# Kernel optimization log

Hardware: AMD Instinct MI355X
Metric: run time of the kernel (lower is better)

## Reference

```python
import jax, jax.numpy as jnp
import numpy as np

D_MODEL = 512
N_HEADS = 8
D_K = D_MODEL // N_HEADS


def setup_inputs() -> dict:
    key = jax.random.key(0)
    ks = jax.random.split(key, 11)
    B, L, D = 2, 4096, D_MODEL
    s = 1.0 / np.sqrt(D)
    return {
        "q": jax.random.normal(ks[0], (B, L, D), jnp.float32),
        "k": jax.random.normal(ks[1], (B, L, D), jnp.float32),
        "v": jax.random.normal(ks[2], (B, L, D), jnp.float32),
        "Wq": jax.random.normal(ks[3], (D, D), jnp.float32) * s,
        "bq": jnp.zeros((D,), jnp.float32),
        "Wk": jax.random.normal(ks[4], (D, D), jnp.float32) * s,
        "bk": jnp.zeros((D,), jnp.float32),
        "Wv": jax.random.normal(ks[5], (D, D), jnp.float32) * s,
        "bv": jnp.zeros((D,), jnp.float32),
        "Wo": jax.random.normal(ks[6], (D, D), jnp.float32) * s,
        "bo": jnp.zeros((D,), jnp.float32),
    }


def reference(q, k, v, Wq, bq, Wk, bk, Wv, bv, Wo, bo):
    B, L, D = q.shape
    H, dk = N_HEADS, D_K
    # projections -> [B, H, L, dk]
    qh = (q @ Wq + bq).reshape(B, L, H, dk).transpose(0, 2, 1, 3)
    kh = (k @ Wk + bk).reshape(B, -1, H, dk).transpose(0, 2, 1, 3)
    vh = (v @ Wv + bv).reshape(B, -1, H, dk).transpose(0, 2, 1, 3)
    scores = jnp.einsum("bhqd,bhkd->bhqk", qh, kh) / jnp.sqrt(jnp.float32(dk))
    attn = jax.nn.softmax(scores, axis=-1)  # dropout: eval-mode identity
    ctx = jnp.einsum("bhqk,bhkd->bhqd", attn, vh)
    ctx = ctx.transpose(0, 2, 1, 3).reshape(B, L, D)
    return ctx @ Wo + bo
```

## Files before the change

kernel.cpp:

```cpp
#include <hip/hip_runtime.h>
#include <hip/hip_bf16.h>

#define NB 2
#define NL 4096
#define ND 512
#define NH 8
#define NDK 64
#define NM (NB * NL)
#define QSCALE 0.18033688011112042f

typedef short bf16x8_t __attribute__((ext_vector_type(8)));
typedef float f32x4_t __attribute__((ext_vector_type(4)));

static __device__ __forceinline__ unsigned short f2bs(float f) {
  union { float f; unsigned u; } c; c.f = f;
  unsigned r = c.u + 0x7fffu + ((c.u >> 16) & 1u);
  return (unsigned short)(r >> 16);
}
static __device__ __forceinline__ float bs2f(unsigned short s) {
  union { unsigned u; float f; } c; c.u = ((unsigned)s) << 16; return c.f;
}
static __device__ __forceinline__ unsigned pk_bf16(float a, float b) {
  union { __hip_bfloat162 h; unsigned u; } c;
  c.h = __float22bfloat162_rn(make_float2(a, b));
  return c.u;
}
static __device__ __forceinline__ unsigned cvt_pk_hw(float a, float b) {
  unsigned r;
  asm("v_cvt_pk_bf16_f32 %0, %1, %2" : "=v"(r) : "v"(a), "v"(b));
  return r;
}

__global__ __launch_bounds__(256)
void round3_kernel(const float* __restrict__ s0, const float* __restrict__ s1,
                   const float* __restrict__ s2, unsigned short* __restrict__ d0,
                   unsigned short* __restrict__ d1, unsigned short* __restrict__ d2)
{
  const float* s = blockIdx.y == 0 ? s0 : (blockIdx.y == 1 ? s1 : s2);
  unsigned short* d = blockIdx.y == 0 ? d0 : (blockIdx.y == 1 ? d1 : d2);
  const size_t i = ((size_t)blockIdx.x * 256 + threadIdx.x) * 8;
  const float4 f0 = *(const float4*)(s + i);
  const float4 f1 = *(const float4*)(s + i + 4);
  uint4 o;
  o.x = pk_bf16(f0.x, f0.y);
  o.y = pk_bf16(f0.z, f0.w);
  o.z = pk_bf16(f1.x, f1.y);
  o.w = pk_bf16(f1.z, f1.w);
  *(uint4*)(d + i) = o;
}

struct WArgs {
  const float* W[4];
  unsigned short* Th[4];
  unsigned short* Tl[4];
};
__global__ __launch_bounds__(256)
void wsplit_kernel(WArgs a)
{
  const int z = blockIdx.z;
  const float* __restrict__ W = a.W[z];
  const int tid = threadIdx.x;
  const int n = blockIdx.x * 64 + (tid & 63);
  const int kb = blockIdx.y * 64 + (tid >> 6) * 16;
  unsigned short h[16], l[16];
#pragma unroll
  for (int u = 0; u < 16; ++u) {
    const float x = W[(size_t)(kb + u) * ND + n];
    h[u] = f2bs(x);
    l[u] = f2bs(x - bs2f(h[u]));
  }
  unsigned wh[8], wl[8];
#pragma unroll
  for (int p = 0; p < 8; ++p) {
    wh[p] = (unsigned)h[2 * p] | ((unsigned)h[2 * p + 1] << 16);
    wl[p] = (unsigned)l[2 * p] | ((unsigned)l[2 * p + 1] << 16);
  }
  unsigned short* th = a.Th[z] + (size_t)n * ND + kb;
  unsigned short* tl = a.Tl[z] + (size_t)n * ND + kb;
  *(uint4*)th = make_uint4(wh[0], wh[1], wh[2], wh[3]);
  *(uint4*)(th + 8) = make_uint4(wh[4], wh[5], wh[6], wh[7]);
  *(uint4*)tl = make_uint4(wl[0], wl[1], wl[2], wl[3]);
  *(uint4*)(tl + 8) = make_uint4(wl[4], wl[5], wl[6], wl[7]);
}

template <bool ASPLIT, int NJ, int OUTMODE>
__device__ __forceinline__ void gemm_core(
    const unsigned short* __restrict__ Ahi, const unsigned short* __restrict__ Alo,
    const unsigned short* __restrict__ Bh, const unsigned short* __restrict__ Bl,
    const float* __restrict__ bias, unsigned short* __restrict__ outH,
    float* __restrict__ outF, int m0, int n0, float scale)
{
  __shared__ unsigned short AH[128][36];
  __shared__ unsigned short AL[ASPLIT ? 128 : 1][36];
  __shared__ unsigned short BHs[NJ * 16][36];
  __shared__ unsigned short BLs[NJ * 16][36];

  const int tid = threadIdx.x;
  const int lane = tid & 63, w = tid >> 6;
  const int m = lane & 15, quad = lane >> 4;
  const int r = tid >> 1, hf = (tid & 1) * 16;
  const int rb = (NJ == 8) ? (tid >> 1) : (tid >> 2);
  const int cb = (NJ == 8) ? ((tid & 1) * 16) : ((tid & 3) * 8);

  const unsigned short* aRow = Ahi + (size_t)(m0 + r) * ND + hf;
  const unsigned short* alRow = ASPLIT ? (Alo + (size_t)(m0 + r) * ND + hf) : nullptr;
  const unsigned short* bhRow = Bh + (size_t)(n0 + rb) * ND + cb;
  const unsigned short* blRow = Bl + (size_t)(n0 + rb) * ND + cb;

  uint4 ra0 = *(const uint4*)(aRow);
  uint4 ra1 = *(const uint4*)(aRow + 8);
  uint4 rl0, rl1;
  if constexpr (ASPLIT) {
    rl0 = *(const uint4*)(alRow);
    rl1 = *(const uint4*)(alRow + 8);
  }
  uint4 rbh0 = *(const uint4*)(bhRow);
  uint4 rbl0 = *(const uint4*)(blRow);
  uint4 rbh1, rbl1;
  if constexpr (NJ == 8) {
    rbh1 = *(const uint4*)(bhRow + 8);
    rbl1 = *(const uint4*)(blRow + 8);
  }

  f32x4_t acc[2][NJ];
#pragma unroll
  for (int i = 0; i < 2; ++i)
#pragma unroll
    for (int j = 0; j < NJ; ++j) acc[i][j] = (f32x4_t){0.f, 0.f, 0.f, 0.f};

  for (int k0 = 0; k0 < ND; k0 += 32) {
    __syncthreads();
    *(uint4*)&AH[r][hf] = ra0;
    *(uint4*)&AH[r][hf + 8] = ra1;
    if constexpr (ASPLIT) {
      *(uint4*)&AL[r][hf] = rl0;
      *(uint4*)&AL[r][hf + 8] = rl1;
    }
    *(uint4*)&BHs[rb][cb] = rbh0;
    *(uint4*)&BLs[rb][cb] = rbl0;
    if constexpr (NJ == 8) {
      *(uint4*)&BHs[rb][cb + 8] = rbh1;
      *(uint4*)&BLs[rb][cb + 8] = rbl1;
    }
    if (k0 + 32 < ND) {
      const int kn = k0 + 32;
      ra0 = *(const uint4*)(aRow + kn);
      ra1 = *(const uint4*)(aRow + kn + 8);
      if constexpr (ASPLIT) {
        rl0 = *(const uint4*)(alRow + kn);
        rl1 = *(const uint4*)(alRow + kn + 8);
      }
      rbh0 = *(const uint4*)(bhRow + kn);
      rbl0 = *(const uint4*)(blRow + kn);
      if constexpr (NJ == 8) {
        rbh1 = *(const uint4*)(bhRow + kn + 8);
        rbl1 = *(const uint4*)(blRow + kn + 8);
      }
    }
    __syncthreads();

    bf16x8_t ah[2], al[2];
#pragma unroll
    for (int i = 0; i < 2; ++i) {
      ah[i] = *(const bf16x8_t*)&AH[w * 32 + 16 * i + m][quad * 8];
      if constexpr (ASPLIT) al[i] = *(const bf16x8_t*)&AL[w * 32 + 16 * i + m][quad * 8];
    }
#pragma unroll
    for (int j = 0; j < NJ; ++j) {
      const bf16x8_t bhj = *(const bf16x8_t*)&BHs[16 * j + m][quad * 8];
      const bf16x8_t blj = *(const bf16x8_t*)&BLs[16 * j + m][quad * 8];
#pragma unroll
      for (int i = 0; i < 2; ++i) {
        acc[i][j] = __builtin_amdgcn_mfma_f32_16x16x32_bf16(ah[i], bhj, acc[i][j], 0, 0, 0);
        acc[i][j] = __builtin_amdgcn_mfma_f32_16x16x32_bf16(ah[i], blj, acc[i][j], 0, 0, 0);
        if constexpr (ASPLIT)
          acc[i][j] = __builtin_amdgcn_mfma_f32_16x16x32_bf16(al[i], bhj, acc[i][j], 0, 0, 0);
      }
    }
  }

  if constexpr (OUTMODE == 1) {
#pragma unroll
    for (int i = 0; i < 2; ++i)
#pragma unroll
      for (int rr = 0; rr < 4; ++rr) {
        const int mg = m0 + w * 32 + 16 * i + quad * 4 + rr;
#pragma unroll
        for (int j = 0; j < NJ; ++j) {
          const int n = n0 + 16 * j + m;
          outF[(size_t)mg * ND + n] = (acc[i][j][rr] + bias[n]) * scale;
        }
      }
  } else if constexpr (OUTMODE == 0) {
    unsigned short* T = &BHs[0][0];
    const int bb = m0 >> 12;
#pragma unroll 1
    for (int p = 0; p < 4; ++p) {
      __syncthreads();
      if (w == p) {
#pragma unroll
        for (int i = 0; i < 2; ++i)
#pragma unroll
          for (int j = 0; j < NJ; ++j) {
            const int n = 16 * j + m;
            const float bv = bias[n0 + n];
#pragma unroll
            for (int rr = 0; rr < 4; ++rr)
              T[(16 * i + quad * 4 + rr) * 136 + n] =
                  f2bs((acc[i][j][rr] + bv) * scale);
          }
      }
      __syncthreads();
      const int lr = tid >> 3;
      const int seg = tid & 7;
      const uint4 t0 = *(const uint4*)&T[lr * 136 + seg * 16];
      const uint4 t1 = *(const uint4*)&T[lr * 136 + seg * 16 + 8];
      const int ng = n0 + seg * 16;
      const int h = ng >> 6, d = ng & (NDK - 1);
      const int l = (m0 + p * 32 + lr) & (NL - 1);
      unsigned short* dp = outH + (((size_t)(bb * NH + h)) * NL + l) * NDK + d;
      *(uint4*)dp = t0;
      *(uint4*)(dp + 8) = t1;
    }
  } else {
    unsigned short* T = &BHs[0][0];
    const int bb = m0 >> 12;
    const int lbase = m0 & (NL - 1);
#pragma unroll 1
    for (int p = 0; p < 4; ++p) {
      __syncthreads();
      if (w == p) {
#pragma unroll
        for (int i = 0; i < 2; ++i)
#pragma unroll
          for (int j = 0; j < NJ; ++j) {
            const int n = 16 * j + m;
            const float bv = bias[n0 + n];
            const unsigned w0 = pk_bf16((acc[i][j][0] + bv) * scale,
                                        (acc[i][j][1] + bv) * scale);
            const unsigned w1 = pk_bf16((acc[i][j][2] + bv) * scale,
                                        (acc[i][j][3] + bv) * scale);
            *(uint2*)&T[n * 34 + 16 * i + quad * 4] = make_uint2(w0, w1);
          }
      }
      __syncthreads();
      const int n = tid >> 1;
      const int l0 = (tid & 1) * 16;
      const uint4 t0 = *(const uint4*)&T[n * 34 + l0];
      const uint4 t1 = *(const uint4*)&T[n * 34 + l0 + 8];
      const int ng = n0 + n;
      const int h = ng >> 6, d = ng & (NDK - 1);
      unsigned short* dp =
          outH + (((size_t)(bb * NH + h)) * NDK + d) * NL + lbase + 32 * p + l0;
      *(uint4*)dp = t0;
      *(uint4*)(dp + 8) = t1;
    }
  }
}

struct ProjArgs {
  const unsigned short* A[3];
  const unsigned short* Bh[3];
  const unsigned short* Bl[3];
  const float* bias[3];
  unsigned short* out[3];
  float scale[3];
};
__global__ __launch_bounds__(256, 3)
void gemm_proj_kernel(ProjArgs a)
{
  const int z = blockIdx.z;
  if (z < 2)
    gemm_core<false, 8, 0>(a.A[z], nullptr, a.Bh[z], a.Bl[z], a.bias[z], a.out[z],
                           nullptr, blockIdx.x * 128, blockIdx.y * 128, a.scale[z]);
  else
    gemm_core<false, 8, 2>(a.A[2], nullptr, a.Bh[2], a.Bl[2], a.bias[2], a.out[2],
                           nullptr, blockIdx.x * 128, blockIdx.y * 128, a.scale[2]);
}
__global__ __launch_bounds__(256, 3)
void gemm_out_kernel(const unsigned short* __restrict__ Ahi,
                     const unsigned short* __restrict__ Alo,
                     const unsigned short* __restrict__ Bh,
                     const unsigned short* __restrict__ Bl,
                     const float* __restrict__ bias, float* __restrict__ out)
{
  gemm_core<true, 4, 1>(Ahi, Alo, Bh, Bl, bias, nullptr, out,
                        blockIdx.x * 128, blockIdx.y * 64, 1.0f);
}

__global__ __launch_bounds__(256, 2)
void attn_kernel(const unsigned short* __restrict__ qh, const unsigned short* __restrict__ kh,
                 const unsigned short* __restrict__ vt_g, float* __restrict__ op,
                 float* __restrict__ lp)
{
  __shared__ unsigned short Ks[2][64 * 64];
  __shared__ unsigned short Vt[2][64 * 64];

  const int tid = threadIdx.x;
  const int w = tid >> 6;
  const int lane = tid & 63;
  const int m = lane & 15;
  const int quad = lane >> 4;
  const int sw = m & 7;

  const int bid = blockIdx.x;
  const int half = bid & 1;
  const int qt = (bid >> 1) & 15;
  const int bh = bid >> 5;
  const int kt0 = half * 32, kt1 = kt0 + 32;
  const unsigned short* qb = qh + (size_t)bh * NL * NDK;
  const unsigned short* kb = kh + (size_t)bh * NL * NDK;
  const unsigned short* vb = vt_g + (size_t)bh * NDK * NL;

  bf16x8_t aq[4][2];
#pragma unroll
  for (int mt = 0; mt < 4; ++mt) {
    const unsigned short* qsrc =
        qb + (size_t)(qt * 256 + w * 64 + mt * 16 + m) * NDK + quad * 8;
    aq[mt][0] = *(const bf16x8_t*)(qsrc);
    aq[mt][1] = *(const bf16x8_t*)(qsrc + 32);
  }

  const short ob = (short)0x3F80;
  const bf16x8_t ones = {ob, ob, ob, ob, ob, ob, ob, ob};

  f32x4_t o[4][4];
#pragma unroll
  for (int mt = 0; mt < 4; ++mt)
#pragma unroll
    for (int nt = 0; nt < 4; ++nt) o[mt][nt] = (f32x4_t){0.f, 0.f, 0.f, 0.f};
  f32x4_t ol[4];
#pragma unroll
  for (int mt = 0; mt < 4; ++mt) ol[mt] = (f32x4_t){0.f, 0.f, 0.f, 0.f};

  const int kr = tid >> 2;
  const int kcb = tid & 3;
  const int kc = kcb * 16;
  const int r7 = kr & 7;
  const int st0 = kr * 64 + ((2 * kcb) ^ r7) * 8;
  const int st1 = kr * 64 + ((2 * kcb + 1) ^ r7) * 8;

  const int rowb = m * 64;
  const int ck0 = rowb + ((quad ^ sw) * 8);
  const int ck1 = rowb + (((quad + 4) ^ sw) * 8);
  const int vq = quad >> 1, vo = (quad & 1) * 4;
  const int va0[2] = { rowb + vo + (((0 + vq) ^ sw) * 8),
                       rowb + vo + (((4 + vq) ^ sw) * 8) };
  const int va1[2] = { rowb + vo + (((2 + vq) ^ sw) * 8),
                       rowb + vo + (((6 + vq) ^ sw) * 8) };

  const unsigned short* kptr = kb + (size_t)(kt0 * 64 + kr) * NDK + kc;
  const unsigned short* vptr = vb + (size_t)kr * NL + kt0 * 64 + kc;
  uint4 pk0 = *(const uint4*)kptr;
  uint4 pk1 = *(const uint4*)(kptr + 8);
  uint4 pv0 = *(const uint4*)vptr;
  uint4 pv1 = *(const uint4*)(vptr + 8);
  *(uint4*)&Ks[0][st0] = pk0;
  *(uint4*)&Ks[0][st1] = pk1;
  *(uint4*)&Vt[0][st0] = pv0;
  *(uint4*)&Vt[0][st1] = pv1;
  kptr += 64 * NDK;
  vptr += 64;
  pk0 = *(const uint4*)kptr;
  pk1 = *(const uint4*)(kptr + 8);
  pv0 = *(const uint4*)vptr;
  pv1 = *(const uint4*)(vptr + 8);
  __syncthreads();

#define ATTN_STEP(B, W, KT)                                                   \
  {                                                                           \
            \
    f32x4_t s[4][4];                                            \
    _Pragma("unroll")                                                         \
    for (int nt = 0; nt < 4; ++nt) {                                          \
      const bf16x8_t kf0 = *(const bf16x8_t*)&Ks[B][nt * 1024 + ck0];         \
      const bf16x8_t kf1 = *(const bf16x8_t*)&Ks[B][nt * 1024 + ck1];         \
      _Pragma("unroll")                                                       \
      for (int mt = 0; mt < 4; ++mt) {                                        \
        f32x4_t s_ = (f32x4_t){0.f, 0.f, 0.f, 0.f};                           \
        s_ = __builtin_amdgcn_mfma_f32_16x16x32_bf16(kf0, aq[mt][0], s_, 0, 0, 0); \
        s_ = __builtin_amdgcn_mfma_f32_16x16x32_bf16(kf1, aq[mt][1], s_, 0, 0, 0); \
        s[nt][mt] = s_;                                                       \
      }                                                                       \
    }                                                                         \
    __builtin_amdgcn_sched_barrier(0);   \
    _Pragma("unroll")                                                         \
    for (int c = 0; c < 2; ++c) {                                             \
      union U { bf16x8_t v; unsigned d[4]; };                                 \
      U pa[4];                                                                \
      _Pragma("unroll")                                                       \
      for (int mt = 0; mt < 4; ++mt) {                                        \
        pa[mt].d[0] = cvt_pk_hw(__builtin_amdgcn_exp2f(s[2 * c][mt][0]),      \
                                __builtin_amdgcn_exp2f(s[2 * c][mt][1]));     \
        pa[mt].d[1] = cvt_pk_hw(__builtin_amdgcn_exp2f(s[2 * c][mt][2]),      \
                                __builtin_amdgcn_exp2f(s[2 * c][mt][3]));     \
        pa[mt].d[2] = cvt_pk_hw(__builtin_amdgcn_exp2f(s[2 * c + 1][mt][0]),  \
                                __builtin_amdgcn_exp2f(s[2 * c + 1][mt][1])); \
        pa[mt].d[3] = cvt_pk_hw(__builtin_amdgcn_exp2f(s[2 * c + 1][mt][2]),  \
                                __builtin_amdgcn_exp2f(s[2 * c + 1][mt][3])); \
      }                                                                       \
      __builtin_amdgcn_s_setprio(1);                                          \
      _Pragma("unroll")                                                       \
      for (int nt = 0; nt < 4; ++nt) {                                        \
        union { bf16x8_t v; uint2 h[2]; } vf;                                 \
        vf.h[0] = *(const uint2*)&Vt[B][nt * 1024 + va0[c]];                  \
        vf.h[1] = *(const uint2*)&Vt[B][nt * 1024 + va1[c]];                  \
        _Pragma("unroll")                                                     \
        for (int mt = 0; mt < 4; ++mt)                                        \
          o[mt][nt] = __builtin_amdgcn_mfma_f32_16x16x32_bf16(pa[mt].v, vf.v, \
                                                              o[mt][nt], 0, 0, 0); \
      }                                                                       \
      _Pragma("unroll")                                                       \
      for (int mt = 0; mt < 4; ++mt)                                          \
        ol[mt] = __builtin_amdgcn_mfma_f32_16x16x32_bf16(pa[mt].v, ones,      \
                                                         ol[mt], 0, 0, 0);    \
      __builtin_amdgcn_s_setprio(0);                                          \
    }                                                                         \
    if ((KT) + 1 < kt1) {                                                     \
      *(uint4*)&Ks[W][st0] = pk0;                                             \
      *(uint4*)&Ks[W][st1] = pk1;                                             \
      *(uint4*)&Vt[W][st0] = pv0;                                             \
      *(uint4*)&Vt[W][st1] = pv1;                                             \
      if ((KT) + 2 < kt1) {                                                   \
        kptr += 64 * NDK;                                                     \
        vptr += 64;                                                           \
        pk0 = *(const uint4*)kptr;                                            \
        pk1 = *(const uint4*)(kptr + 8);                                      \
        pv0 = *(const uint4*)vptr;                                            \
        pv1 = *(const uint4*)(vptr + 8);                                      \
      }                                                                       \
      __syncthreads();                                                        \
    }                                                                         \
  }

  for (int kt = kt0; kt < kt1; kt += 2) {
    ATTN_STEP(0, 1, kt);
    ATTN_STEP(1, 0, kt + 1);
  }
#undef ATTN_STEP

  const size_t pbase = (size_t)(half * 16 + bh) * NL;
#pragma unroll
  for (int mt = 0; mt < 4; ++mt) {
    const int q0 = qt * 256 + w * 64 + mt * 16 + quad * 4;
    if (m == 0)
      *(float4*)&lp[pbase + q0] =
          make_float4(ol[mt][0], ol[mt][1], ol[mt][2], ol[mt][3]);
#pragma unroll
    for (int r = 0; r < 4; ++r) {
      float* dst = op + (pbase + q0 + r) * NDK;
#pragma unroll
      for (int nt = 0; nt < 4; ++nt) dst[16 * nt + m] = o[mt][nt][r];
    }
  }
}

__global__ __launch_bounds__(256)
void merge_kernel(const float* __restrict__ op, const float* __restrict__ lp,
                  unsigned short* __restrict__ ctxh, unsigned short* __restrict__ ctxl)
{
  const size_t t = (size_t)blockIdx.x * 256 + threadIdx.x;
  const int d0 = (int)(t & 7) * 8;
  const size_t row = t >> 3;
  const float l0 = lp[row];
  const float l1 = lp[row + (size_t)16 * NL];
  const float inv = 1.0f / (l0 + l1);
  const float* a = op + row * NDK + d0;
  const float* c = a + (size_t)16 * NL * NDK;
  const float4 a0 = *(const float4*)a, a1 = *(const float4*)(a + 4);
  const float4 c0 = *(const float4*)c, c1 = *(const float4*)(c + 4);
  const float x[8] = {(a0.x + c0.x) * inv, (a0.y + c0.y) * inv,
                      (a0.z + c0.z) * inv, (a0.w + c0.w) * inv,
                      (a1.x + c1.x) * inv, (a1.y + c1.y) * inv,
                      (a1.z + c1.z) * inv, (a1.w + c1.w) * inv};
  unsigned short hs[8], ls[8];
#pragma unroll
  for (int u = 0; u < 8; ++u) {
    hs[u] = f2bs(x[u]);
    ls[u] = f2bs(x[u] - bs2f(hs[u]));
  }
  const int bh = (int)(row >> 12), l = (int)(row & (NL - 1));
  const int b = bh >> 3, h = bh & 7;
  const size_t dst = ((size_t)(b * NL + l)) * ND + h * 64 + d0;
  uint4 uh, ul;
  uh.x = (unsigned)hs[0] | ((unsigned)hs[1] << 16);
  uh.y = (unsigned)hs[2] | ((unsigned)hs[3] << 16);
  uh.z = (unsigned)hs[4] | ((unsigned)hs[5] << 16);
  uh.w = (unsigned)hs[6] | ((unsigned)hs[7] << 16);
  ul.x = (unsigned)ls[0] | ((unsigned)ls[1] << 16);
  ul.y = (unsigned)ls[2] | ((unsigned)ls[3] << 16);
  ul.z = (unsigned)ls[4] | ((unsigned)ls[5] << 16);
  ul.w = (unsigned)ls[6] | ((unsigned)ls[7] << 16);
  *(uint4*)(ctxh + dst) = uh;
  *(uint4*)(ctxl + dst) = ul;
}

extern "C" void kernel_launch(void* const* d_in, const int* in_sizes, int n_in,
                              void* d_out, int out_size, void* d_ws, size_t ws_size,
                              hipStream_t stream)
{
  const float* q  = (const float*)d_in[0];
  const float* k  = (const float*)d_in[1];
  const float* v  = (const float*)d_in[2];
  const float* Wq = (const float*)d_in[3];
  const float* bq = (const float*)d_in[4];
  const float* Wk = (const float*)d_in[5];
  const float* bk = (const float*)d_in[6];
  const float* Wv = (const float*)d_in[7];
  const float* bv = (const float*)d_in[8];
  const float* Wo = (const float*)d_in[9];
  const float* bo = (const float*)d_in[10];

  const size_t PLANE = (size_t)NM * ND;
  unsigned short* wt = (unsigned short*)d_ws;
  unsigned short* qhp = wt + 8 * (size_t)ND * ND;
  unsigned short* khp = qhp + PLANE;
  unsigned short* vtp = khp + PLANE;
  float* op = (float*)(vtp + PLANE);
  float* lp = op + 2 * (size_t)16 * NL * NDK;
  unsigned short* qb = (unsigned short*)op;
  unsigned short* kb = qb + PLANE;
  unsigned short* vb = kb + PLANE;
  unsigned short* ctxh = qhp;
  unsigned short* ctxl = khp;

  unsigned short* wth[4], *wtl[4];
  for (int i = 0; i < 4; ++i) {
    wth[i] = wt + (size_t)(2 * i) * ND * ND;
    wtl[i] = wt + (size_t)(2 * i + 1) * ND * ND;
  }

  round3_kernel<<<dim3(PLANE / (256 * 8), 3), 256, 0, stream>>>(q, k, v, qb, kb, vb);

  WArgs wa;
  wa.W[0] = Wq; wa.W[1] = Wk; wa.W[2] = Wv; wa.W[3] = Wo;
  for (int i = 0; i < 4; ++i) { wa.Th[i] = wth[i]; wa.Tl[i] = wtl[i]; }
  wsplit_kernel<<<dim3(8, 8, 4), 256, 0, stream>>>(wa);

  ProjArgs pa;
  pa.A[0] = qb; pa.A[1] = kb; pa.A[2] = vb;
  pa.Bh[0] = wth[0]; pa.Bl[0] = wtl[0];
  pa.Bh[1] = wth[1]; pa.Bl[1] = wtl[1];
  pa.Bh[2] = wth[2]; pa.Bl[2] = wtl[2];
  pa.bias[0] = bq; pa.bias[1] = bk; pa.bias[2] = bv;
  pa.out[0] = qhp; pa.out[1] = khp; pa.out[2] = vtp;
  pa.scale[0] = QSCALE; pa.scale[1] = 1.0f; pa.scale[2] = 1.0f;
  gemm_proj_kernel<<<dim3(NM / 128, ND / 128, 3), 256, 0, stream>>>(pa);

  attn_kernel<<<dim3(NB * NH * (NL / 256) * 2), 256, 0, stream>>>(qhp, khp, vtp, op, lp);

  merge_kernel<<<dim3((16 * NL * NDK) / (256 * 8)), 256, 0, stream>>>(op, lp, ctxh, ctxl);

  gemm_out_kernel<<<dim3(NM / 128, ND / 64), 256, 0, stream>>>(
      ctxh, ctxl, wth[3], wtl[3], bo, (float*)d_out);
}
```

Baseline: 242.9 us.

## Fuse fp32-to-bf16 input conversion into projection GEMM and use 2x2 wave grid

```diff
diff --git a/kernel.cpp b/kernel.cpp
--- a/kernel.cpp
+++ b/kernel.cpp
@@ -31,24 +31,6 @@
   return r;
 }
 
-__global__ __launch_bounds__(256)
-void round3_kernel(const float* __restrict__ s0, const float* __restrict__ s1,
-                   const float* __restrict__ s2, unsigned short* __restrict__ d0,
-                   unsigned short* __restrict__ d1, unsigned short* __restrict__ d2)
-{
-  const float* s = blockIdx.y == 0 ? s0 : (blockIdx.y == 1 ? s1 : s2);
-  unsigned short* d = blockIdx.y == 0 ? d0 : (blockIdx.y == 1 ? d1 : d2);
-  const size_t i = ((size_t)blockIdx.x * 256 + threadIdx.x) * 8;
-  const float4 f0 = *(const float4*)(s + i);
-  const float4 f1 = *(const float4*)(s + i + 4);
-  uint4 o;
-  o.x = pk_bf16(f0.x, f0.y);
-  o.y = pk_bf16(f0.z, f0.w);
-  o.z = pk_bf16(f1.x, f1.y);
-  o.w = pk_bf16(f1.z, f1.w);
-  *(uint4*)(d + i) = o;
-}
-
 struct WArgs {
   const float* W[4];
   unsigned short* Th[4];
@@ -83,13 +65,19 @@
   *(uint4*)(tl + 8) = make_uint4(wl[4], wl[5], wl[6], wl[7]);
 }
 
-template <bool ASPLIT, int NJ, int OUTMODE>
+template <bool ASPLIT, int NJ, int OUTMODE, int WI, int WJ, bool AFP32>
 __device__ __forceinline__ void gemm_core(
-    const unsigned short* __restrict__ Ahi, const unsigned short* __restrict__ Alo,
+    const void* __restrict__ Ahi_, const unsigned short* __restrict__ Alo,
     const unsigned short* __restrict__ Bh, const unsigned short* __restrict__ Bl,
     const float* __restrict__ bias, unsigned short* __restrict__ outH,
     float* __restrict__ outF, int m0, int n0, float scale)
 {
+  static_assert(!(ASPLIT && AFP32), "unsupported combo");
+  constexpr int WGC = NJ / WJ;
+  static_assert((4 / WGC) * WI * 16 == 128, "wave grid must tile 128 rows");
+  static_assert(OUTMODE == 1 || (WI == 4 && WJ == 4 && WGC == 2),
+                "epilogues 0/2 assume 2x2 wave grid");
+
   __shared__ unsigned short AH[128][36];
   __shared__ unsigned short AL[ASPLIT ? 128 : 1][36];
   __shared__ unsigned short BHs[NJ * 16][36];
@@ -98,17 +86,32 @@
   const int tid = threadIdx.x;
   const int lane = tid & 63, w = tid >> 6;
   const int m = lane & 15, quad = lane >> 4;
+  const int wr = w / WGC, wc = w % WGC;
   const int r = tid >> 1, hf = (tid & 1) * 16;
   const int rb = (NJ == 8) ? (tid >> 1) : (tid >> 2);
   const int cb = (NJ == 8) ? ((tid & 1) * 16) : ((tid & 3) * 8);
 
-  const unsigned short* aRow = Ahi + (size_t)(m0 + r) * ND + hf;
+  const unsigned short* aRow = nullptr;
+  const float* aRowF = nullptr;
+  if constexpr (AFP32)
+    aRowF = (const float*)Ahi_ + (size_t)(m0 + r) * ND + hf;
+  else
+    aRow = (const unsigned short*)Ahi_ + (size_t)(m0 + r) * ND + hf;
   const unsigned short* alRow = ASPLIT ? (Alo + (size_t)(m0 + r) * ND + hf) : nullptr;
   const unsigned short* bhRow = Bh + (size_t)(n0 + rb) * ND + cb;
   const unsigned short* blRow = Bl + (size_t)(n0 + rb) * ND + cb;
 
-  uint4 ra0 = *(const uint4*)(aRow);
-  uint4 ra1 = *(const uint4*)(aRow + 8);
+  uint4 ra0, ra1;
+  float4 fa[4];
+  if constexpr (AFP32) {
+    fa[0] = *(const float4*)(aRowF);
+    fa[1] = *(const float4*)(aRowF + 4);
+    fa[2] = *(const float4*)(aRowF + 8);
+    fa[3] = *(const float4*)(aRowF + 12);
+  } else {
+    ra0 = *(const uint4*)(aRow);
+    ra1 = *(const uint4*)(aRow + 8);
+  }
   uint4 rl0, rl1;
   if constexpr (ASPLIT) {
     rl0 = *(const uint4*)(alRow);
@@ -122,16 +125,30 @@
     rbl1 = *(const uint4*)(blRow + 8);
   }
 
-  f32x4_t acc[2][NJ];
-#pragma unroll
-  for (int i = 0; i < 2; ++i)
-#pragma unroll
-    for (int j = 0; j < NJ; ++j) acc[i][j] = (f32x4_t){0.f, 0.f, 0.f, 0.f};
+  f32x4_t acc[WI][WJ];
+#pragma unroll
+  for (int i = 0; i < WI; ++i)
+#pragma unroll
+    for (int j = 0; j < WJ; ++j) acc[i][j] = (f32x4_t){0.f, 0.f, 0.f, 0.f};
 
   for (int k0 = 0; k0 < ND; k0 += 32) {
     __syncthreads();
-    *(uint4*)&AH[r][hf] = ra0;
-    *(uint4*)&AH[r][hf + 8] = ra1;
+    if constexpr (AFP32) {
+      uint4 ua0, ua1;
+      ua0.x = pk_bf16(fa[0].x, fa[0].y);
+      ua0.y = pk_bf16(fa[0].z, fa[0].w);
+      ua0.z = pk_bf16(fa[1].x, fa[1].y);
+      ua0.w = pk_bf16(fa[1].z, fa[1].w);
+      ua1.x = pk_bf16(fa[2].x, fa[2].y);
+      ua1.y = pk_bf16(fa[2].z, fa[2].w);
+      ua1.z = pk_bf16(fa[3].x, fa[3].y);
+      ua1.w = pk_bf16(fa[3].z, fa[3].w);
+      *(uint4*)&AH[r][hf] = ua0;
+      *(uint4*)&AH[r][hf + 8] = ua1;
+    } else {
+      *(uint4*)&AH[r][hf] = ra0;
+      *(uint4*)&AH[r][hf + 8] = ra1;
+    }
     if constexpr (ASPLIT) {
       *(uint4*)&AL[r][hf] = rl0;
       *(uint4*)&AL[r][hf + 8] = rl1;
@@ -144,8 +161,15 @@
     }
     if (k0 + 32 < ND) {
       const int kn = k0 + 32;
-      ra0 = *(const uint4*)(aRow + kn);
-      ra1 = *(const uint4*)(aRow + kn + 8);
+      if constexpr (AFP32) {
+        fa[0] = *(const float4*)(aRowF + kn);
+        fa[1] = *(const float4*)(aRowF + kn + 4);
+        fa[2] = *(const float4*)(aRowF + kn + 8);
+        fa[3] = *(const float4*)(aRowF + kn + 12);
+      } else {
+        ra0 = *(const uint4*)(aRow + kn);
+        ra1 = *(const uint4*)(aRow + kn + 8);
+      }
       if constexpr (ASPLIT) {
         rl0 = *(const uint4*)(alRow + kn);
         rl1 = *(const uint4*)(alRow + kn + 8);
@@ -159,18 +183,19 @@
     }
     __syncthreads();
 
-    bf16x8_t ah[2], al[2];
-#pragma unroll
-    for (int i = 0; i < 2; ++i) {
-      ah[i] = *(const bf16x8_t*)&AH[w * 32 + 16 * i + m][quad * 8];
-      if constexpr (ASPLIT) al[i] = *(const bf16x8_t*)&AL[w * 32 + 16 * i + m][quad * 8];
-    }
-#pragma unroll
-    for (int j = 0; j < NJ; ++j) {
-      const bf16x8_t bhj = *(const bf16x8_t*)&BHs[16 * j + m][quad * 8];
-      const bf16x8_t blj = *(const bf16x8_t*)&BLs[16 * j + m][quad * 8];
-#pragma unroll
-      for (int i = 0; i < 2; ++i) {
+    bf16x8_t ah[WI], al[ASPLIT ? WI : 1];
+#pragma unroll
+    for (int i = 0; i < WI; ++i) {
+      ah[i] = *(const bf16x8_t*)&AH[wr * (WI * 16) + 16 * i + m][quad * 8];
+      if constexpr (ASPLIT)
+        al[i] = *(const bf16x8_t*)&AL[wr * (WI * 16) + 16 * i + m][quad * 8];
+    }
+#pragma unroll
+    for (int j = 0; j < WJ; ++j) {
+      const bf16x8_t bhj = *(const bf16x8_t*)&BHs[16 * (wc * WJ + j) + m][quad * 8];
+      const bf16x8_t blj = *(const bf16x8_t*)&BLs[16 * (wc * WJ + j) + m][quad * 8];
+#pragma unroll
+      for (int i = 0; i < WI; ++i) {
         acc[i][j] = __builtin_amdgcn_mfma_f32_16x16x32_bf16(ah[i], bhj, acc[i][j], 0, 0, 0);
         acc[i][j] = __builtin_amdgcn_mfma_f32_16x16x32_bf16(ah[i], blj, acc[i][j], 0, 0, 0);
         if constexpr (ASPLIT)
@@ -181,13 +206,13 @@
 
   if constexpr (OUTMODE == 1) {
 #pragma unroll
-    for (int i = 0; i < 2; ++i)
+    for (int i = 0; i < WI; ++i)
 #pragma unroll
       for (int rr = 0; rr < 4; ++rr) {
-        const int mg = m0 + w * 32 + 16 * i + quad * 4 + rr;
-#pragma unroll
-        for (int j = 0; j < NJ; ++j) {
-          const int n = n0 + 16 * j + m;
+        const int mg = m0 + wr * (WI * 16) + 16 * i + quad * 4 + rr;
+#pragma unroll
+        for (int j = 0; j < WJ; ++j) {
+          const int n = n0 + 16 * (wc * WJ + j) + m;
           outF[(size_t)mg * ND + n] = (acc[i][j][rr] + bias[n]) * scale;
         }
       }
@@ -197,18 +222,20 @@
 #pragma unroll 1
     for (int p = 0; p < 4; ++p) {
       __syncthreads();
-      if (w == p) {
-#pragma unroll
-        for (int i = 0; i < 2; ++i)
-#pragma unroll
-          for (int j = 0; j < NJ; ++j) {
-            const int n = 16 * j + m;
+      if (wr == (p >> 1)) {
+#pragma unroll
+        for (int i2 = 0; i2 < 2; ++i2) {
+          const int i = (p & 1) * 2 + i2;
+#pragma unroll
+          for (int j = 0; j < WJ; ++j) {
+            const int n = wc * 64 + 16 * j + m;
             const float bv = bias[n0 + n];
 #pragma unroll
             for (int rr = 0; rr < 4; ++rr)
-              T[(16 * i + quad * 4 + rr) * 136 + n] =
+              T[(16 * i2 + quad * 4 + rr) * 136 + n] =
                   f2bs((acc[i][j][rr] + bv) * scale);
           }
+        }
       }
       __syncthreads();
       const int lr = tid >> 3;
@@ -229,19 +256,21 @@
 #pragma unroll 1
     for (int p = 0; p < 4; ++p) {
       __syncthreads();
-      if (w == p) {
-#pragma unroll
-        for (int i = 0; i < 2; ++i)
-#pragma unroll
-          for (int j = 0; j < NJ; ++j) {
-            const int n = 16 * j + m;
+      if (wr == (p >> 1)) {
+#pragma unroll
+        for (int i2 = 0; i2 < 2; ++i2) {
+          const int i = (p & 1) * 2 + i2;
+#pragma unroll
+          for (int j = 0; j < WJ; ++j) {
+            const int n = wc * 64 + 16 * j + m;
             const float bv = bias[n0 + n];
             const unsigned w0 = pk_bf16((acc[i][j][0] + bv) * scale,
                                         (acc[i][j][1] + bv) * scale);
             const unsigned w1 = pk_bf16((acc[i][j][2] + bv) * scale,
                                         (acc[i][j][3] + bv) * scale);
-            *(uint2*)&T[n * 34 + 16 * i + quad * 4] = make_uint2(w0, w1);
+            *(uint2*)&T[n * 34 + 16 * i2 + quad * 4] = make_uint2(w0, w1);
           }
+        }
       }
       __syncthreads();
       const int n = tid >> 1;
@@ -259,7 +288,7 @@
 }
 
 struct ProjArgs {
-  const unsigned short* A[3];
+  const float* A[3];
   const unsigned short* Bh[3];
   const unsigned short* Bl[3];
   const float* bias[3];
@@ -271,11 +300,13 @@
 {
   const int z = blockIdx.z;
   if (z < 2)
-    gemm_core<false, 8, 0>(a.A[z], nullptr, a.Bh[z], a.Bl[z], a.bias[z], a.out[z],
-                           nullptr, blockIdx.x * 128, blockIdx.y * 128, a.scale[z]);
+    gemm_core<false, 8, 0, 4, 4, true>(a.A[z], nullptr, a.Bh[z], a.Bl[z],
+                                       a.bias[z], a.out[z], nullptr,
+                                       blockIdx.x * 128, blockIdx.y * 128, a.scale[z]);
   else
-    gemm_core<false, 8, 2>(a.A[2], nullptr, a.Bh[2], a.Bl[2], a.bias[2], a.out[2],
-                           nullptr, blockIdx.x * 128, blockIdx.y * 128, a.scale[2]);
+    gemm_core<false, 8, 2, 4, 4, true>(a.A[2], nullptr, a.Bh[2], a.Bl[2],
+                                       a.bias[2], a.out[2], nullptr,
+                                       blockIdx.x * 128, blockIdx.y * 128, a.scale[2]);
 }
 __global__ __launch_bounds__(256, 3)
 void gemm_out_kernel(const unsigned short* __restrict__ Ahi,
@@ -284,8 +315,8 @@
                      const unsigned short* __restrict__ Bl,
                      const float* __restrict__ bias, float* __restrict__ out)
 {
-  gemm_core<true, 4, 1>(Ahi, Alo, Bh, Bl, bias, nullptr, out,
-                        blockIdx.x * 128, blockIdx.y * 64, 1.0f);
+  gemm_core<true, 4, 1, 2, 4, false>(Ahi, Alo, Bh, Bl, bias, nullptr, out,
+                                     blockIdx.x * 128, blockIdx.y * 64, 1.0f);
 }
 
 __global__ __launch_bounds__(256, 2)
@@ -518,9 +549,6 @@
   unsigned short* vtp = khp + PLANE;
   float* op = (float*)(vtp + PLANE);
   float* lp = op + 2 * (size_t)16 * NL * NDK;
-  unsigned short* qb = (unsigned short*)op;
-  unsigned short* kb = qb + PLANE;
-  unsigned short* vb = kb + PLANE;
   unsigned short* ctxh = qhp;
   unsigned short* ctxl = khp;
 
@@ -530,15 +558,13 @@
     wtl[i] = wt + (size_t)(2 * i + 1) * ND * ND;
   }
 
-  round3_kernel<<<dim3(PLANE / (256 * 8), 3), 256, 0, stream>>>(q, k, v, qb, kb, vb);
-
   WArgs wa;
   wa.W[0] = Wq; wa.W[1] = Wk; wa.W[2] = Wv; wa.W[3] = Wo;
   for (int i = 0; i < 4; ++i) { wa.Th[i] = wth[i]; wa.Tl[i] = wtl[i]; }
   wsplit_kernel<<<dim3(8, 8, 4), 256, 0, stream>>>(wa);
 
   ProjArgs pa;
-  pa.A[0] = qb; pa.A[1] = kb; pa.A[2] = vb;
+  pa.A[0] = q; pa.A[1] = k; pa.A[2] = v;
   pa.Bh[0] = wth[0]; pa.Bl[0] = wtl[0];
   pa.Bh[1] = wth[1]; pa.Bl[1] = wtl[1];
   pa.Bh[2] = wth[2]; pa.Bl[2] = wtl[2];
```

After: 388.2 us. 59.8% more time.
